# Kernel optimization log

Measured on AMD Instinct MI355X. Metric: run time of the kernel, lower is better.

## Reference

```python
import jax, jax.numpy as jnp
import numpy as np

# dims / constants (from init_kwargs and ParamsHP defaults)
N, C, TRS, SPT, BUF = 800, 64, 40, 10, 120
DT = 1e-4                      # step_size
A, OMEGA, G = -0.5, 10.0, 500.0
STD_IN, CY0, Y0_OFF, KG, KI = 100.0, 5.0, 2.0, 5.0, 1.0
T = TRS * SPT                  # total integration steps


def setup_inputs() -> dict:
    key = jax.random.key(0)
    k = jax.random.split(key, 7)
    external = jax.random.normal(k[0], (N, SPT, TRS), dtype=jnp.float32)
    hx = jax.random.uniform(k[1], (N, 2), dtype=jnp.float32)
    hE = jax.random.uniform(k[2], (N, BUF), dtype=jnp.float32)
    sc = jax.random.uniform(k[3], (N, N), dtype=jnp.float32)
    lm = jax.random.normal(k[4], (C, N), dtype=jnp.float32)
    noise_in = jax.random.normal(k[5], (T, N, 2), dtype=jnp.float32)
    # delays[i,j] = int(dist[i,j] / mu), bounded by buffer length
    delays = jax.random.randint(k[6], (N, N), 0, BUF, dtype=jnp.int64)
    return {"external": external, "hx": hx, "hE": hE, "sc": sc,
            "lm": lm, "noise_in": noise_in, "delays": delays}


def reference(external, hx, hE, sc, lm, noise_in, delays):
    # normalized structural connectivity and Laplacian diagonal term
    w = jnp.abs(sc)
    w_n = w / jnp.linalg.norm(w)          # (N,N)
    rowsum = jnp.sum(w_n, axis=1)         # (N,) -> dg = -diag(rowsum)
    jcol = jnp.broadcast_to(jnp.arange(N)[None, :], (N, N))
    # stimulus as (T, N): external is (N, steps_per_TR, TRs_per_window)
    ext = jnp.transpose(external, (2, 1, 0)).reshape(T, N)
    sqdt = jnp.sqrt(DT)

    def step(carry, inp):
        x, y, hEb = carry                 # x,y: (N,), hEb: (N,BUF)
        u, ns = inp                       # u: (N,), ns: (N,2)
        # delayed activity: Ed[i,j] = x_j(t - delays[i,j])
        Ed = hEb[jcol, delays]            # (N,N) irregular gather
        LEd = jnp.sum(w_n * Ed, axis=1)   # connectivity-weighted coupling
        r2 = x * x + y * y
        dx = (A - r2) * x - OMEGA * y + G * (LEd - rowsum * x) + KG * KI * u
        dy = (A - r2) * y + OMEGA * x
        x_new = x + DT * dx + sqdt * STD_IN * ns[:, 0]
        y_new = y + DT * dy + sqdt * STD_IN * ns[:, 1]
        hEb = jnp.concatenate([x_new[:, None], hEb[:, :-1]], axis=1)
        return (x_new, y_new, hEb), x_new

    (xf, yf, hEf), xs = jax.lax.scan(step, (hx[:, 0], hx[:, 1], hE), (ext, noise_in))
    # one EEG sample per TR (state at the last step of each TR)
    x_tr = xs.reshape(TRS, SPT, N)[:, -1, :]   # (TRS, N)
    eeg = CY0 * (x_tr @ lm.T) - Y0_OFF          # leadfield projection (TRS, C)
    return eeg.T                                # (C, TRS)
```

## Files before the change

### kernel.cpp

```cpp
#include <hip/hip_runtime.h>
#include <hip/hip_cooperative_groups.h>

namespace cg = cooperative_groups;

#define N_      800
#define C_      64
#define TRS_    40
#define SPT_    10
#define BUF_    120
#define T_      400
#define STRIDE  528
#define KPL     13
#define SENT    0x7FC00BADu
#define NEAR_D  15

#define A_F     (-0.5f)
#define OMEGA_F (10.0f)
#define G_F     (500.0f)
#define KGI_F   (5.0f)
#define DT_F    (1e-4f)

#define ALD(p)    __hip_atomic_load((p), __ATOMIC_RELAXED, __HIP_MEMORY_SCOPE_AGENT)
#define AST(p,v)  __hip_atomic_store((p), (v), __ATOMIC_RELAXED, __HIP_MEMORY_SCOPE_AGENT)


__global__ void k_sumsq(const float* __restrict__ sc, float* __restrict__ sumsq) {
    __shared__ float sh[4];
    int tid = threadIdx.x;
    int idx = blockIdx.x * 256 + tid;
    float s = 0.f;
    for (int i = idx; i < N_ * N_; i += 256 * 256) { float v = sc[i]; s += v * v; }
    #pragma unroll
    for (int o = 1; o < 64; o <<= 1) s += __shfl_xor(s, o, 64);
    if ((tid & 63) == 0) sh[tid >> 6] = s;
    __syncthreads();
    if (tid == 0) atomicAdd(sumsq, sh[0] + sh[1] + sh[2] + sh[3]);
}

__global__ void k_detect(const int* __restrict__ dw, int* __restrict__ flag) {
    __shared__ int sh[4];
    int tid = threadIdx.x;
    int v = 0;
    for (int idx = 2 * tid + 1; idx < 800; idx += 512) v |= dw[idx];
    #pragma unroll
    for (int o = 1; o < 64; o <<= 1) v |= __shfl_xor(v, o, 64);
    if ((tid & 63) == 0) sh[tid >> 6] = v;
    __syncthreads();
    if (tid == 0) flag[0] = ((sh[0] | sh[1] | sh[2] | sh[3]) == 0) ? 1 : 0;
}

__global__ void k_init(const float* __restrict__ hE, unsigned int* __restrict__ xh) {
    int idx = blockIdx.x * 256 + threadIdx.x;
    if (idx >= N_ * 520) return;
    int j = idx / 520, s = idx - j * 520;
    unsigned int v = (s < 120) ? __float_as_uint(hE[j * BUF_ + (119 - s)]) : SENT;
    xh[j * STRIDE + s] = v;
}


__global__ void __launch_bounds__(512, 1) k_main(
    const float* __restrict__ sc, const int* __restrict__ dw,
    const float* __restrict__ hx, const float* __restrict__ external,
    const float* __restrict__ noise, const float* __restrict__ lm,
    const float* __restrict__ sumsq, const int* __restrict__ flag,
    unsigned int* __restrict__ xh, float* __restrict__ xtr, float* __restrict__ out)
{
    cg::grid_group grid = cg::this_grid();
    const int lane = threadIdx.x & 63;
    const int i = (int)((blockIdx.x * 512 + threadIdx.x) >> 6);

    const float inv_norm = 1.0f / sqrtf(*sumsq);
    const int is64 = *flag;

    float wn[KPL], wf[KPL]; int an[KPL], af[KPL];
    float rsum = 0.f;
    #pragma unroll
    for (int k = 0; k < KPL; ++k) {
        int j = k * 64 + lane;
        bool valid = (j < N_);
        int jj = valid ? j : 0;
        int base = i * N_ + jj;
        float wv = valid ? fabsf(sc[base]) * inv_norm : 0.f;
        int dv = valid ? dw[is64 ? (base << 1) : base] : 119;
        rsum += wv;
        bool nearc = valid && (dv < NEAR_D);
        bool farc  = valid && (dv >= NEAR_D);
        wn[k] = nearc ? wv : 0.f;
        wf[k] = farc  ? wv : 0.f;
        an[k] = jj * STRIDE + 119 - (nearc ? dv : 119);
        af[k] = jj * STRIDE + 119 - (farc  ? dv : 119);
    }
    #pragma unroll
    for (int o = 1; o < 64; o <<= 1) rsum += __shfl_xor(rsum, o, 64);

    float x = hx[2 * i], y = hx[2 * i + 1];

    #pragma unroll 1
    for (int mb = 0; mb < 25; ++mb) {
        const int t0 = mb * 16;

        float fps[16];
        #pragma unroll
        for (int s = 0; s < 16; ++s) fps[s] = 0.f;

        #pragma unroll
        for (int k = 0; k < KPL; ++k) {
            bool fm = (wf[k] != 0.f);
            int a = af[k] + t0;
            int p = a & 3;
            int A = a - p;
            float4 q0, q1, q2, q3, q4;
            if (fm) {
                const float4* f4 = reinterpret_cast<const float4*>((const float*)xh + A);
                q0 = f4[0]; q1 = f4[1]; q2 = f4[2]; q3 = f4[3]; q4 = f4[4];
            } else {
                q0 = q1 = q2 = q3 = q4 = make_float4(0.f, 0.f, 0.f, 0.f);
            }
            float win[20] = { q0.x,q0.y,q0.z,q0.w, q1.x,q1.y,q1.z,q1.w,
                              q2.x,q2.y,q2.z,q2.w, q3.x,q3.y,q3.z,q3.w,
                              q4.x,q4.y,q4.z,q4.w };
            int g = 0;
            while (true) {
                int pend = 0;
                #pragma unroll
                for (int z = 0; z < 20; ++z)
                    pend |= (int)((z >= p) & (z < p + 16) &
                                  (__float_as_uint(win[z]) == SENT));
                if (!__any(pend)) break;
                if (++g > 1000000) break;
                #pragma unroll
                for (int z = 0; z < 20; ++z)
                    if ((z >= p) && (z < p + 16) && __float_as_uint(win[z]) == SENT)
                        win[z] = __uint_as_float(ALD(&xh[A + z]));
            }
            float wk = wf[k];
            #pragma unroll
            for (int s = 0; s < 16; ++s) {
                float v01 = (p & 1) ? win[s + 1] : win[s];
                float v23 = (p & 1) ? win[s + 3] : win[s + 2];
                float v   = (p & 2) ? v23 : v01;
                fps[s] += wk * v;
            }
        }

        #pragma unroll
        for (int s = 0; s < 16; ++s) {
            const int t = t0 + s;
            int tr = (t * 205) >> 11;
            int sp = t - tr * 10;
            float u  = external[(i * SPT_ + sp) * TRS_ + tr];
            float n0 = noise[(t * N_ + i) * 2 + 0];
            float n1 = noise[(t * N_ + i) * 2 + 1];

            unsigned vv[KPL];
            #pragma unroll
            for (int k = 0; k < KPL; ++k)
                vv[k] = (wn[k] != 0.f) ? ALD(&xh[an[k] + t]) : 0u;
            int g = 0;
            while (true) {
                int pend = 0;
                #pragma unroll
                for (int k = 0; k < KPL; ++k) pend |= (vv[k] == SENT) ? 1 : 0;
                if (!__any(pend)) break;
                if (++g > 1000000) break;
                #pragma unroll
                for (int k = 0; k < KPL; ++k)
                    if (vv[k] == SENT) vv[k] = ALD(&xh[an[k] + t]);
            }
            float acc = fps[s];
            #pragma unroll
            for (int k = 0; k < KPL; ++k) acc += wn[k] * __uint_as_float(vv[k]);
            #pragma unroll
            for (int o = 1; o < 64; o <<= 1) acc += __shfl_xor(acc, o, 64);

            float r2 = x * x + y * y;
            float dx = (A_F - r2) * x - OMEGA_F * y + G_F * (acc - rsum * x) + KGI_F * u;
            float dy = (A_F - r2) * y + OMEGA_F * x;
            x = x + DT_F * dx + n0;
            y = y + DT_F * dy + n1;

            if (lane == 0) {
                AST(&xh[i * STRIDE + 120 + t], __float_as_uint(x));
                if (sp == SPT_ - 1) xtr[tr * N_ + i] = x;
            }
        }
    }

    grid.sync();

    for (int o = i; o < C_ * TRS_; o += 800) {
        int c = o / TRS_, tr = o - c * TRS_;
        float s = 0.f;
        #pragma unroll
        for (int k = 0; k < KPL; ++k) {
            int n = k * 64 + lane;
            if (n < N_) s += xtr[tr * N_ + n] * lm[c * N_ + n];
        }
        #pragma unroll
        for (int o2 = 1; o2 < 64; o2 <<= 1) s += __shfl_xor(s, o2, 64);
        if (lane == 0) out[o] = 5.0f * s - 2.0f;
    }
}


extern "C" void kernel_launch(void* const* d_in, const int* in_sizes, int n_in,
                              void* d_out, int out_size, void* d_ws, size_t ws_size,
                              hipStream_t stream) {
    const float* external = (const float*)d_in[0];
    const float* hx       = (const float*)d_in[1];
    const float* hE       = (const float*)d_in[2];
    const float* sc       = (const float*)d_in[3];
    const float* lm       = (const float*)d_in[4];
    const float* noise    = (const float*)d_in[5];
    const int*   delays   = (const int*)  d_in[6];
    float* out = (float*)d_out;

    float*        sumsq = (float*)d_ws;
    int*          flag  = (int*)d_ws + 1;
    unsigned int* xh    = (unsigned int*)d_ws + 64;
    float*        xtr   = (float*)(xh + N_ * STRIDE);

    hipMemsetAsync(d_ws, 0, 8, stream);
    k_sumsq<<<256, 256, 0, stream>>>(sc, sumsq);
    k_detect<<<1, 256, 0, stream>>>(delays, flag);
    k_init<<<(N_ * 520 + 255) / 256, 256, 0, stream>>>(hE, xh);

    void* args[] = { (void*)&sc, (void*)&delays, (void*)&hx, (void*)&external,
                     (void*)&noise, (void*)&lm, (void*)&sumsq, (void*)&flag,
                     (void*)&xh, (void*)&xtr, (void*)&out };
    hipLaunchCooperativeKernel((const void*)k_main, dim3(100), dim3(512), args, 0, stream);
}
```

Baseline: 2.729 ms.

## Switch delayed coupling to push-based scatter into per-row LDS ring buffers

Reorganises the coupling sum from a pull-style gather over each row's delayed history into a push-style scatter. After each step, every block fetches the full new state vector into LDS and atomically adds w_ij*x_j into a per-row ring buffer at slot t+1+delay. The history is stored time-major so each step's row can be polled coalesced. This removes the per-step scattered global gathers and the wavefront reduction, and only one time row is polled per step. The cost is a block-wide __syncthreads each step and up to 13 LDS atomic adds per lane per step, which may contend on the same ring slots.

```diff
diff --git a/kernel.cpp b/kernel.cpp
--- a/kernel.cpp
+++ b/kernel.cpp
@@ -7,12 +7,10 @@
 #define C_      64
 #define TRS_    40
 #define SPT_    10
-#define BUF_    120
 #define T_      400
-#define STRIDE  528
+#define HIST_   520
 #define KPL     13
 #define SENT    0x7FC00BADu
-#define NEAR_D  15
 
 #define A_F     (-0.5f)
 #define OMEGA_F (10.0f)
@@ -49,12 +47,12 @@
     if (tid == 0) flag[0] = ((sh[0] | sh[1] | sh[2] | sh[3]) == 0) ? 1 : 0;
 }
 
-__global__ void k_init(const float* __restrict__ hE, unsigned int* __restrict__ xh) {
+__global__ void k_init(const float* __restrict__ hE, unsigned int* __restrict__ xg) {
     int idx = blockIdx.x * 256 + threadIdx.x;
-    if (idx >= N_ * 520) return;
-    int j = idx / 520, s = idx - j * 520;
-    unsigned int v = (s < 120) ? __float_as_uint(hE[j * BUF_ + (119 - s)]) : SENT;
-    xh[j * STRIDE + s] = v;
+    if (idx >= HIST_ * N_) return;
+    int s = idx / N_, j = idx - s * N_;
+    unsigned int v = (s < 120) ? __float_as_uint(hE[j * 120 + (119 - s)]) : SENT;
+    xg[idx] = v;
 }
 
 
@@ -63,16 +61,21 @@
     const float* __restrict__ hx, const float* __restrict__ external,
     const float* __restrict__ noise, const float* __restrict__ lm,
     const float* __restrict__ sumsq, const int* __restrict__ flag,
-    unsigned int* __restrict__ xh, float* __restrict__ xtr, float* __restrict__ out)
+    unsigned int* __restrict__ xg, float* __restrict__ xtr, float* __restrict__ out)
 {
     cg::grid_group grid = cg::this_grid();
+    __shared__ float xsh[2][N_];
+    __shared__ float ring[8][128];
+
     const int lane = threadIdx.x & 63;
-    const int i = (int)((blockIdx.x * 512 + threadIdx.x) >> 6);
+    const int wid  = threadIdx.x >> 6;
+    const int i    = blockIdx.x * 8 + wid;
+    const int B0   = blockIdx.x * 8;
 
     const float inv_norm = 1.0f / sqrtf(*sumsq);
     const int is64 = *flag;
 
-    float wn[KPL], wf[KPL]; int an[KPL], af[KPL];
+    float w[KPL]; int dl[KPL];
     float rsum = 0.f;
     #pragma unroll
     for (int k = 0; k < KPL; ++k) {
@@ -81,107 +84,76 @@
         int jj = valid ? j : 0;
         int base = i * N_ + jj;
         float wv = valid ? fabsf(sc[base]) * inv_norm : 0.f;
-        int dv = valid ? dw[is64 ? (base << 1) : base] : 119;
+        dl[k] = valid ? dw[is64 ? (base << 1) : base] : 0;
+        w[k]  = wv;
         rsum += wv;
-        bool nearc = valid && (dv < NEAR_D);
-        bool farc  = valid && (dv >= NEAR_D);
-        wn[k] = nearc ? wv : 0.f;
-        wf[k] = farc  ? wv : 0.f;
-        an[k] = jj * STRIDE + 119 - (nearc ? dv : 119);
-        af[k] = jj * STRIDE + 119 - (farc  ? dv : 119);
     }
     #pragma unroll
     for (int o = 1; o < 64; o <<= 1) rsum += __shfl_xor(rsum, o, 64);
 
+    ring[wid][lane] = 0.f;
+    ring[wid][64 + lane] = 0.f;
+
     float x = hx[2 * i], y = hx[2 * i + 1];
 
     #pragma unroll 1
-    for (int mb = 0; mb < 25; ++mb) {
-        const int t0 = mb * 16;
-
-        float fps[16];
-        #pragma unroll
-        for (int s = 0; s < 16; ++s) fps[s] = 0.f;
-
+    for (int s = 0; s < 120; ++s) {
         #pragma unroll
         for (int k = 0; k < KPL; ++k) {
-            bool fm = (wf[k] != 0.f);
-            int a = af[k] + t0;
-            int p = a & 3;
-            int A = a - p;
-            float4 q0, q1, q2, q3, q4;
-            if (fm) {
-                const float4* f4 = reinterpret_cast<const float4*>((const float*)xh + A);
-                q0 = f4[0]; q1 = f4[1]; q2 = f4[2]; q3 = f4[3]; q4 = f4[4];
-            } else {
-                q0 = q1 = q2 = q3 = q4 = make_float4(0.f, 0.f, 0.f, 0.f);
+            if (w[k] != 0.f) {
+                float v = __uint_as_float(xg[s * N_ + k * 64 + lane]);
+                int tt = s - 119 + dl[k];
+                if (tt >= 0) atomicAdd(&ring[wid][tt & 127], w[k] * v);
             }
-            float win[20] = { q0.x,q0.y,q0.z,q0.w, q1.x,q1.y,q1.z,q1.w,
-                              q2.x,q2.y,q2.z,q2.w, q3.x,q3.y,q3.z,q3.w,
-                              q4.x,q4.y,q4.z,q4.w };
-            int g = 0;
-            while (true) {
-                int pend = 0;
-                #pragma unroll
-                for (int z = 0; z < 20; ++z)
-                    pend |= (int)((z >= p) & (z < p + 16) &
-                                  (__float_as_uint(win[z]) == SENT));
-                if (!__any(pend)) break;
-                if (++g > 1000000) break;
-                #pragma unroll
-                for (int z = 0; z < 20; ++z)
-                    if ((z >= p) && (z < p + 16) && __float_as_uint(win[z]) == SENT)
-                        win[z] = __uint_as_float(ALD(&xh[A + z]));
-            }
-            float wk = wf[k];
-            #pragma unroll
-            for (int s = 0; s < 16; ++s) {
-                float v01 = (p & 1) ? win[s + 1] : win[s];
-                float v23 = (p & 1) ? win[s + 3] : win[s + 2];
-                float v   = (p & 2) ? v23 : v01;
-                fps[s] += wk * v;
-            }
-        }
-
-        #pragma unroll
-        for (int s = 0; s < 16; ++s) {
-            const int t = t0 + s;
-            int tr = (t * 205) >> 11;
-            int sp = t - tr * 10;
-            float u  = external[(i * SPT_ + sp) * TRS_ + tr];
-            float n0 = noise[(t * N_ + i) * 2 + 0];
-            float n1 = noise[(t * N_ + i) * 2 + 1];
-
-            unsigned vv[KPL];
-            #pragma unroll
-            for (int k = 0; k < KPL; ++k)
-                vv[k] = (wn[k] != 0.f) ? ALD(&xh[an[k] + t]) : 0u;
-            int g = 0;
-            while (true) {
-                int pend = 0;
-                #pragma unroll
-                for (int k = 0; k < KPL; ++k) pend |= (vv[k] == SENT) ? 1 : 0;
-                if (!__any(pend)) break;
-                if (++g > 1000000) break;
-                #pragma unroll
-                for (int k = 0; k < KPL; ++k)
-                    if (vv[k] == SENT) vv[k] = ALD(&xh[an[k] + t]);
-            }
-            float acc = fps[s];
-            #pragma unroll
-            for (int k = 0; k < KPL; ++k) acc += wn[k] * __uint_as_float(vv[k]);
-            #pragma unroll
-            for (int o = 1; o < 64; o <<= 1) acc += __shfl_xor(acc, o, 64);
-
-            float r2 = x * x + y * y;
-            float dx = (A_F - r2) * x - OMEGA_F * y + G_F * (acc - rsum * x) + KGI_F * u;
-            float dy = (A_F - r2) * y + OMEGA_F * x;
-            x = x + DT_F * dx + n0;
-            y = y + DT_F * dy + n1;
-
-            if (lane == 0) {
-                AST(&xh[i * STRIDE + 120 + t], __float_as_uint(x));
-                if (sp == SPT_ - 1) xtr[tr * N_ + i] = x;
+        }
+    }
+
+    #pragma unroll 1
+    for (int t = 0; t < T_; ++t) {
+        float led = ring[wid][t & 127];
+        if (lane == 0) ring[wid][t & 127] = 0.f;
+
+        int tr = (t * 205) >> 11;
+        int sp = t - tr * 10;
+        float u  = external[(i * SPT_ + sp) * TRS_ + tr];
+        float n0 = noise[(t * N_ + i) * 2 + 0];
+        float n1 = noise[(t * N_ + i) * 2 + 1];
+
+        float r2 = x * x + y * y;
+        float dx = (A_F - r2) * x - OMEGA_F * y + G_F * (led - rsum * x) + KGI_F * u;
+        float dy = (A_F - r2) * y + OMEGA_F * x;
+        x = x + DT_F * dx + n0;
+        y = y + DT_F * dy + n1;
+
+        int par = t & 1;
+        unsigned int* Xrow = xg + (120 + t) * N_;
+        if (lane == 0) {
+            AST(&Xrow[i], __float_as_uint(x));
+            xsh[par][i] = x;
+            if (sp == SPT_ - 1) xtr[tr * N_ + i] = x;
+        }
+
+        int j0 = wid * 100 + lane;
+        int j1 = j0 + 64;
+        bool m0 = !(j0 >= B0 && j0 < B0 + 8);
+        bool m1 = (lane < 36) && !(j1 >= B0 && j1 < B0 + 8);
+        unsigned int v0 = m0 ? ALD(&Xrow[j0]) : 0u;
+        unsigned int v1 = m1 ? ALD(&Xrow[j1]) : 0u;
+        int g = 0;
+        while (__any((v0 == SENT) || (v1 == SENT))) {
+            if (++g > 1000000) break;
+            if (v0 == SENT) v0 = ALD(&Xrow[j0]);
+            if (v1 == SENT) v1 = ALD(&Xrow[j1]);
+        }
+        if (m0) xsh[par][j0] = __uint_as_float(v0);
+        if (m1) xsh[par][j1] = __uint_as_float(v1);
+        __syncthreads();
+
+        #pragma unroll
+        for (int k = 0; k < KPL; ++k) {
+            if (w[k] != 0.f) {
+                float v = xsh[par][k * 64 + lane];
+                atomicAdd(&ring[wid][(t + 1 + dl[k]) & 127], w[k] * v);
             }
         }
     }
@@ -217,16 +189,16 @@
 
     float*        sumsq = (float*)d_ws;
     int*          flag  = (int*)d_ws + 1;
-    unsigned int* xh    = (unsigned int*)d_ws + 64;
-    float*        xtr   = (float*)(xh + N_ * STRIDE);
+    unsigned int* xg    = (unsigned int*)d_ws + 64;
+    float*        xtr   = (float*)(xg + HIST_ * N_);
 
     hipMemsetAsync(d_ws, 0, 8, stream);
     k_sumsq<<<256, 256, 0, stream>>>(sc, sumsq);
     k_detect<<<1, 256, 0, stream>>>(delays, flag);
-    k_init<<<(N_ * 520 + 255) / 256, 256, 0, stream>>>(hE, xh);
+    k_init<<<(HIST_ * N_ + 255) / 256, 256, 0, stream>>>(hE, xg);
 
     void* args[] = { (void*)&sc, (void*)&delays, (void*)&hx, (void*)&external,
                      (void*)&noise, (void*)&lm, (void*)&sumsq, (void*)&flag,
-                     (void*)&xh, (void*)&xtr, (void*)&out };
+                     (void*)&xg, (void*)&xtr, (void*)&out };
     hipLaunchCooperativeKernel((const void*)k_main, dim3(100), dim3(512), args, 0, stream);
 }
```

Result: slower. 5.424 ms (+98.8%).

## Split delayed coupling into near/mid/far tiers and stagger block phase per node

Applied to the files above, without the earlier changes.

Delayed connections are split into three tiers instead of two. Far (delay >= 16) terms are prefetched per 16-step block, mid (4-15) per 4-step group, and near (<4) per step. Each node's 16-step block boundary is offset by i&15, so not all waves poll and stall on the same block boundary at once. This aims to spread the spin-wait load across the grid and move more of the gather off the per-step critical path, at the cost of extra bookkeeping, an extra partial loop iteration, and more branching.

```diff
diff --git a/kernel.cpp b/kernel.cpp
--- a/kernel.cpp
+++ b/kernel.cpp
@@ -12,7 +12,8 @@
 #define STRIDE  528
 #define KPL     13
 #define SENT    0x7FC00BADu
-#define NEAR_D  15
+#define NEAR_D  4
+#define MID_D   16
 
 #define A_F     (-0.5f)
 #define OMEGA_F (10.0f)
@@ -72,7 +73,7 @@
     const float inv_norm = 1.0f / sqrtf(*sumsq);
     const int is64 = *flag;
 
-    float wn[KPL], wf[KPL]; int an[KPL], af[KPL];
+    float wn[KPL], wm[KPL], wf[KPL]; int aw[KPL];
     float rsum = 0.f;
     #pragma unroll
     for (int k = 0; k < KPL; ++k) {
@@ -83,105 +84,165 @@
         float wv = valid ? fabsf(sc[base]) * inv_norm : 0.f;
         int dv = valid ? dw[is64 ? (base << 1) : base] : 119;
         rsum += wv;
-        bool nearc = valid && (dv < NEAR_D);
-        bool farc  = valid && (dv >= NEAR_D);
-        wn[k] = nearc ? wv : 0.f;
-        wf[k] = farc  ? wv : 0.f;
-        an[k] = jj * STRIDE + 119 - (nearc ? dv : 119);
-        af[k] = jj * STRIDE + 119 - (farc  ? dv : 119);
+        wn[k] = (valid && dv < NEAR_D) ? wv : 0.f;
+        wm[k] = (valid && dv >= NEAR_D && dv < MID_D) ? wv : 0.f;
+        wf[k] = (valid && dv >= MID_D) ? wv : 0.f;
+        aw[k] = jj * STRIDE + 119 - dv;
     }
     #pragma unroll
     for (int o = 1; o < 64; o <<= 1) rsum += __shfl_xor(rsum, o, 64);
 
     float x = hx[2 * i], y = hx[2 * i + 1];
+    const int p = i & 15;
 
     #pragma unroll 1
-    for (int mb = 0; mb < 25; ++mb) {
-        const int t0 = mb * 16;
+    for (int m = -1; m < 25; ++m) {
+        const int tb = p + 16 * m;
+        const int flo = (tb < 0) ? -tb : 0;
+        const int fhi = (400 - tb < 16) ? (400 - tb) : 16;
 
         float fps[16];
         #pragma unroll
         for (int s = 0; s < 16; ++s) fps[s] = 0.f;
 
-        #pragma unroll
-        for (int k = 0; k < KPL; ++k) {
-            bool fm = (wf[k] != 0.f);
-            int a = af[k] + t0;
-            int p = a & 3;
-            int A = a - p;
-            float4 q0, q1, q2, q3, q4;
-            if (fm) {
-                const float4* f4 = reinterpret_cast<const float4*>((const float*)xh + A);
-                q0 = f4[0]; q1 = f4[1]; q2 = f4[2]; q3 = f4[3]; q4 = f4[4];
-            } else {
-                q0 = q1 = q2 = q3 = q4 = make_float4(0.f, 0.f, 0.f, 0.f);
-            }
-            float win[20] = { q0.x,q0.y,q0.z,q0.w, q1.x,q1.y,q1.z,q1.w,
-                              q2.x,q2.y,q2.z,q2.w, q3.x,q3.y,q3.z,q3.w,
-                              q4.x,q4.y,q4.z,q4.w };
-            int g = 0;
-            while (true) {
-                int pend = 0;
-                #pragma unroll
-                for (int z = 0; z < 20; ++z)
-                    pend |= (int)((z >= p) & (z < p + 16) &
-                                  (__float_as_uint(win[z]) == SENT));
-                if (!__any(pend)) break;
-                if (++g > 1000000) break;
-                #pragma unroll
-                for (int z = 0; z < 20; ++z)
-                    if ((z >= p) && (z < p + 16) && __float_as_uint(win[z]) == SENT)
-                        win[z] = __uint_as_float(ALD(&xh[A + z]));
-            }
-            float wk = wf[k];
+        if (flo < fhi) {
             #pragma unroll
-            for (int s = 0; s < 16; ++s) {
-                float v01 = (p & 1) ? win[s + 1] : win[s];
-                float v23 = (p & 1) ? win[s + 3] : win[s + 2];
-                float v   = (p & 2) ? v23 : v01;
-                fps[s] += wk * v;
+            for (int k = 0; k < KPL; ++k) {
+                bool fm = (wf[k] != 0.f);
+                int a = aw[k] + tb;
+                int pp = a & 3;
+                int A = a - pp;
+                float4 q0, q1, q2, q3, q4;
+                if (fm) {
+                    const float4* f4 = reinterpret_cast<const float4*>((const float*)xh + A);
+                    q0 = f4[0]; q1 = f4[1]; q2 = f4[2]; q3 = f4[3]; q4 = f4[4];
+                } else {
+                    q0 = q1 = q2 = q3 = q4 = make_float4(0.f, 0.f, 0.f, 0.f);
+                }
+                float win[20] = { q0.x,q0.y,q0.z,q0.w, q1.x,q1.y,q1.z,q1.w,
+                                  q2.x,q2.y,q2.z,q2.w, q3.x,q3.y,q3.z,q3.w,
+                                  q4.x,q4.y,q4.z,q4.w };
+                const int zlo = pp + flo, zhi = pp + fhi;
+                int g = 0;
+                while (true) {
+                    int pend = 0;
+                    #pragma unroll
+                    for (int z = 0; z < 20; ++z)
+                        pend |= (int)((z >= zlo) & (z < zhi) &
+                                      (__float_as_uint(win[z]) == SENT));
+                    if (!__any(pend)) break;
+                    if (++g > 1000000) break;
+                    #pragma unroll
+                    for (int z = 0; z < 20; ++z)
+                        if ((z >= zlo) && (z < zhi) && __float_as_uint(win[z]) == SENT)
+                            win[z] = __uint_as_float(ALD(&xh[A + z]));
+                }
+                float wk = wf[k];
+                #pragma unroll
+                for (int s = 0; s < 16; ++s) {
+                    if ((s >= flo) & (s < fhi)) {
+                        float v01 = (pp & 1) ? win[s + 1] : win[s];
+                        float v23 = (pp & 1) ? win[s + 3] : win[s + 2];
+                        float v   = (pp & 2) ? v23 : v01;
+                        fps[s] += wk * v;
+                    }
+                }
             }
         }
 
+        float fm4[4] = {0.f, 0.f, 0.f, 0.f};
+
         #pragma unroll
         for (int s = 0; s < 16; ++s) {
-            const int t = t0 + s;
-            int tr = (t * 205) >> 11;
-            int sp = t - tr * 10;
-            float u  = external[(i * SPT_ + sp) * TRS_ + tr];
-            float n0 = noise[(t * N_ + i) * 2 + 0];
-            float n1 = noise[(t * N_ + i) * 2 + 1];
-
-            unsigned vv[KPL];
-            #pragma unroll
-            for (int k = 0; k < KPL; ++k)
-                vv[k] = (wn[k] != 0.f) ? ALD(&xh[an[k] + t]) : 0u;
-            int g = 0;
-            while (true) {
-                int pend = 0;
-                #pragma unroll
-                for (int k = 0; k < KPL; ++k) pend |= (vv[k] == SENT) ? 1 : 0;
-                if (!__any(pend)) break;
-                if (++g > 1000000) break;
+            const int t = tb + s;
+
+            if ((s & 3) == 0) {
+                if (t + 3 >= 0 && t < 400) {
+                    const int mlo = (t < 0) ? -t : 0;
+                    const int mhi = (400 - t < 4) ? (400 - t) : 4;
+                    #pragma unroll
+                    for (int r = 0; r < 4; ++r) fm4[r] = 0.f;
+                    #pragma unroll
+                    for (int k = 0; k < KPL; ++k) {
+                        bool mm = (wm[k] != 0.f);
+                        int a = aw[k] + t;
+                        int pp = a & 3;
+                        int A = a - pp;
+                        float4 q0, q1;
+                        if (mm) {
+                            const float4* f4 = reinterpret_cast<const float4*>((const float*)xh + A);
+                            q0 = f4[0]; q1 = f4[1];
+                        } else {
+                            q0 = q1 = make_float4(0.f, 0.f, 0.f, 0.f);
+                        }
+                        float win[8] = { q0.x,q0.y,q0.z,q0.w, q1.x,q1.y,q1.z,q1.w };
+                        const int zlo = pp + mlo, zhi = pp + mhi;
+                        int g = 0;
+                        while (true) {
+                            int pend = 0;
+                            #pragma unroll
+                            for (int z = 0; z < 8; ++z)
+                                pend |= (int)((z >= zlo) & (z < zhi) &
+                                              (__float_as_uint(win[z]) == SENT));
+                            if (!__any(pend)) break;
+                            if (++g > 1000000) break;
+                            #pragma unroll
+                            for (int z = 0; z < 8; ++z)
+                                if ((z >= zlo) && (z < zhi) && __float_as_uint(win[z]) == SENT)
+                                    win[z] = __uint_as_float(ALD(&xh[A + z]));
+                        }
+                        float wk = wm[k];
+                        #pragma unroll
+                        for (int r = 0; r < 4; ++r) {
+                            if ((r >= mlo) & (r < mhi)) {
+                                float v01 = (pp & 1) ? win[r + 1] : win[r];
+                                float v23 = (pp & 1) ? win[r + 3] : win[r + 2];
+                                float v   = (pp & 2) ? v23 : v01;
+                                fm4[r] += wk * v;
+                            }
+                        }
+                    }
+                }
+            }
+
+            if (t >= 0 && t < 400) {
+                unsigned int vv[KPL];
                 #pragma unroll
                 for (int k = 0; k < KPL; ++k)
-                    if (vv[k] == SENT) vv[k] = ALD(&xh[an[k] + t]);
-            }
-            float acc = fps[s];
-            #pragma unroll
-            for (int k = 0; k < KPL; ++k) acc += wn[k] * __uint_as_float(vv[k]);
-            #pragma unroll
-            for (int o = 1; o < 64; o <<= 1) acc += __shfl_xor(acc, o, 64);
-
-            float r2 = x * x + y * y;
-            float dx = (A_F - r2) * x - OMEGA_F * y + G_F * (acc - rsum * x) + KGI_F * u;
-            float dy = (A_F - r2) * y + OMEGA_F * x;
-            x = x + DT_F * dx + n0;
-            y = y + DT_F * dy + n1;
-
-            if (lane == 0) {
-                AST(&xh[i * STRIDE + 120 + t], __float_as_uint(x));
-                if (sp == SPT_ - 1) xtr[tr * N_ + i] = x;
+                    vv[k] = (wn[k] != 0.f) ? ALD(&xh[aw[k] + t]) : 0u;
+                int g = 0;
+                while (true) {
+                    int pend = 0;
+                    #pragma unroll
+                    for (int k = 0; k < KPL; ++k) pend |= (vv[k] == SENT) ? 1 : 0;
+                    if (!__any(pend)) break;
+                    if (++g > 1000000) break;
+                    #pragma unroll
+                    for (int k = 0; k < KPL; ++k)
+                        if (vv[k] == SENT) vv[k] = ALD(&xh[aw[k] + t]);
+                }
+                float acc = fps[s] + fm4[s & 3];
+                #pragma unroll
+                for (int k = 0; k < KPL; ++k) acc += wn[k] * __uint_as_float(vv[k]);
+                #pragma unroll
+                for (int o = 1; o < 64; o <<= 1) acc += __shfl_xor(acc, o, 64);
+
+                int tr = (t * 205) >> 11;
+                int sp = t - tr * 10;
+                float u  = external[(i * SPT_ + sp) * TRS_ + tr];
+                float n0 = noise[(t * N_ + i) * 2 + 0];
+                float n1 = noise[(t * N_ + i) * 2 + 1];
+
+                float r2 = x * x + y * y;
+                float dx = (A_F - r2) * x - OMEGA_F * y + G_F * (acc - rsum * x) + KGI_F * u;
+                float dy = (A_F - r2) * y + OMEGA_F * x;
+                x = x + DT_F * dx + n0;
+                y = y + DT_F * dy + n1;
+
+                if (lane == 0) {
+                    AST(&xh[i * STRIDE + 120 + t], __float_as_uint(x));
+                    if (sp == SPT_ - 1) xtr[tr * N_ + i] = x;
+                }
             }
         }
     }
```

Measured after the change: 7.384 ms. +170.6%, slower.
